# Kernel tuning notes

Hardware: AMD Instinct MI355X
Metric: run time of the kernel (lower is better)

Reference implementation:

```python
import jax, jax.numpy as jnp
import numpy as np
from jax import lax

B, T = 2, 2048
D = 512        # d_model
K = 64         # k_lookback (causal window)


def setup_inputs() -> dict:
    key = jax.random.key(0)
    k1, k2, k3 = jax.random.split(key, 3)
    x = jax.random.normal(k1, (B, 1, T), jnp.float32)
    conv_w = jax.random.normal(k2, (D, 1, 3), jnp.float32) * 0.2
    conv_b = jax.random.normal(k3, (D,), jnp.float32) * 0.05
    gate = jnp.array(0.5, jnp.float32)  # nn.Parameter scalar
    return {"x": x, "conv_w": conv_w, "conv_b": conv_b, "gate": gate}


def reference(x, conv_w, conv_b, gate):
    # feature_proj: Conv1d(1, D, k=3, pad=1) + exact GELU (dropout inactive at eval)
    q = lax.conv_general_dilated(
        x, conv_w, window_strides=(1,), padding=[(1, 1)],
        dimension_numbers=("NCH", "OIH", "NCH"))
    q = jax.nn.gelu(q + conv_b[None, :, None], approximate=False)  # [B, D, T]

    # causal sliding windows: keys_windows[b,c,t,j] = q[b,c, t-(K-1)+j] (0 outside)
    padded = jnp.pad(q, ((0, 0), (0, 0), (K - 1, 0)))
    idx = jnp.arange(T)[:, None] + jnp.arange(K)[None, :]  # [T, K]
    kw = padded[:, :, idx]                                  # [B, D, T, K]

    energy = jnp.einsum("bct,bctk->btk", q, kw)             # [B, T, K]
    attn = jax.nn.softmax(energy / np.float32(np.sqrt(D)), axis=-1)
    context = jnp.einsum("btk,bctk->bct", attn, kw)         # [B, D, T]
    return context * jnp.tanh(gate)
```

## Files before the change

kernel.cpp:

```cpp
#include <hip/hip_runtime.h>
#include <math.h>

#define B 2
#define T 2048
#define D 512
#define KW 64
#define SCALE 0.044194173824159216f

typedef __attribute__((ext_vector_type(8))) short short8;
typedef __attribute__((ext_vector_type(4))) float f32x4;

__device__ __forceinline__ ushort f2bf(float f) {
  union { float f; unsigned u; } v; v.f = f;
  unsigned r = v.u + 0x7fffu + ((v.u >> 16) & 1u);
  return (ushort)(r >> 16);
}

__device__ __forceinline__ float gelu_fast(float v) {
  float v2 = v * v;
  float u  = fmaf(v2 * v, 0.03567740814f, 0.7978845608f * v);
  float e  = __builtin_amdgcn_exp2f(2.885390082f * u);
  float r  = __builtin_amdgcn_rcpf(1.f + e);
  return fmaf(-v, r, v);
}

__device__ __forceinline__ int qt_off(int j, int c) {
  return j * 512 + (c ^ ((j & 7) << 3));
}
__device__ __forceinline__ int qc_off(int c, int j) {
  return (j >> 5) * 16384 + c * 32 + ((j & 31) ^ (((c >> 1) & 3) << 3));
}

__global__ __launch_bounds__(256, 1) void k_fused(
    const float* __restrict__ x, const float* __restrict__ w,
    const float* __restrict__ bias, const float* __restrict__ gate,
    float* __restrict__ out) {
  __shared__ alignas(16) ushort s_q[96 * 512];
  __shared__ alignas(16) f32x4 s_E[4 * 5 * 64];
  __shared__ ushort s_attn[4][16 * 96];

  int blk  = blockIdx.x;
  int b    = blk >> 7;
  int t0   = (blk & 127) << 4;
  int tid  = threadIdx.x;
  int wv   = tid >> 6;
  int lane = tid & 63;
  int n    = lane & 15;
  int quad = lane >> 4;

  int c0 = lane * 8;
  float wf[24], bf[8];
#pragma unroll
  for (int v4 = 0; v4 < 6; ++v4)
    *(float4*)&wf[v4 * 4] = *(const float4*)(w + (size_t)c0 * 3 + v4 * 4);
#pragma unroll
  for (int v4 = 0; v4 < 2; ++v4)
    *(float4*)&bf[v4 * 4] = *(const float4*)(bias + c0 + v4 * 4);
  const float* xb = x + (size_t)b * T;

  for (int it = 0; it < 24; ++it) {
    int j  = wv + it * 4;
    int tp = t0 - 64 + j;
    bool inr = (unsigned)tp < (unsigned)T;
    float xm1 = ((unsigned)(tp - 1) < (unsigned)T) ? xb[tp - 1] : 0.f;
    float x0  = inr                    ? xb[tp]     : 0.f;
    float xp1 = ((unsigned)(tp + 1) < (unsigned)T) ? xb[tp + 1] : 0.f;
    short8 pk;
#pragma unroll
    for (int e = 0; e < 8; ++e) {
      float v = fmaf(xm1, wf[e * 3], fmaf(x0, wf[e * 3 + 1],
                fmaf(xp1, wf[e * 3 + 2], bf[e])));
      pk[e] = inr ? (short)f2bf(gelu_fast(v)) : (short)0;
    }
    *(short8*)&s_q[qt_off(j, c0)] = pk;
  }
  __syncthreads();

  short8 afr[4], bfr[4][5];
#pragma unroll
  for (int i = 0; i < 4; ++i) {
    int cofs = (wv * 4 + i) * 32 + quad * 8;
    afr[i] = *(const short8*)&s_q[qt_off(64 + n, cofs)];
#pragma unroll
    for (int jc = 0; jc < 5; ++jc)
      bfr[i][jc] = *(const short8*)&s_q[qt_off(1 + jc * 16 + n, cofs)];
  }

  f32x4 acc[5];
#pragma unroll
  for (int jc = 0; jc < 5; ++jc) acc[jc] = (f32x4){0.f, 0.f, 0.f, 0.f};
#pragma unroll
  for (int i = 0; i < 4; ++i)
#pragma unroll
    for (int jc = 0; jc < 5; ++jc)
      acc[jc] = __builtin_amdgcn_mfma_f32_16x16x32_bf16(afr[i], bfr[i][jc],
                                                        acc[jc], 0, 0, 0);

#pragma unroll
  for (int jc = 0; jc < 5; ++jc)
    s_E[(wv * 5 + jc) * 64 + lane] = acc[jc];
  __syncthreads();

#pragma unroll
  for (int ww = 0; ww < 4; ++ww) {
    if (ww == wv) continue;
#pragma unroll
    for (int jc = 0; jc < 5; ++jc) {
      f32x4 v = s_E[(ww * 5 + jc) * 64 + lane];
      acc[jc][0] += v[0]; acc[jc][1] += v[1];
      acc[jc][2] += v[2]; acc[jc][3] += v[3];
    }
  }

  ushort* sa = s_attn[wv];
#pragma unroll
  for (int r = 0; r < 4; ++r) {
    int m = quad * 4 + r;
    float e[5];
    float mx = -1e30f;
#pragma unroll
    for (int jc = 0; jc < 5; ++jc) {
      int j = jc * 16 + n;
      bool valid = (j >= m) && (j <= m + (KW - 1));
      e[jc] = valid ? acc[jc][r] * SCALE : -1e30f;
      mx = fmaxf(mx, e[jc]);
    }
#pragma unroll
    for (int off = 1; off <= 8; off <<= 1) mx = fmaxf(mx, __shfl_xor(mx, off, 64));
    float p[5];
    float s = 0.f;
#pragma unroll
    for (int jc = 0; jc < 5; ++jc) {
      p[jc] = (e[jc] > -1e29f) ? __expf(e[jc] - mx) : 0.f;
      s += p[jc];
    }
#pragma unroll
    for (int off = 1; off <= 8; off <<= 1) s += __shfl_xor(s, off, 64);
    float inv = 1.f / s;
#pragma unroll
    for (int jc = 0; jc < 5; ++jc) {
      int j = jc * 16 + n;
      sa[m * 96 + j + 1] = f2bf(p[jc] * inv);
    }
    int jp = (n == 0) ? 0 : (80 + n);
    sa[m * 96 + jp] = 0;
  }
  short8 afr2[3];
#pragma unroll
  for (int ks = 0; ks < 3; ++ks)
    afr2[ks] = *(const short8*)(sa + n * 96 + ks * 32 + quad * 8);

  for (int k = 0; k < 3; ++k) {
    short8 tr[8];
#pragma unroll
    for (int g = 0; g < 8; ++g) {
      int c  = tid + ((g & 1) << 8);
      int j0 = (g >> 1) << 3;
#pragma unroll
      for (int e = 0; e < 8; ++e)
        tr[g][e] = (short)s_q[qt_off(k * 32 + j0 + e, c)];
    }
    __syncthreads();
#pragma unroll
    for (int g = 0; g < 8; ++g) {
      int c  = tid + ((g & 1) << 8);
      int j0 = (g >> 1) << 3;
      *(short8*)&s_q[qc_off(c, k * 32 + j0)] = tr[g];
    }
    __syncthreads();
  }

  const float tg = tanhf(gate[0]);
#pragma unroll
  for (int ncl = 0; ncl < 8; ++ncl) {
    int c = (wv * 8 + ncl) * 16 + n;
    f32x4 co = (f32x4){0.f, 0.f, 0.f, 0.f};
#pragma unroll
    for (int ks = 0; ks < 3; ++ks) {
      short8 bfr2 = *(const short8*)&s_q[qc_off(c, ks * 32 + quad * 8)];
      co = __builtin_amdgcn_mfma_f32_16x16x32_bf16(afr2[ks], bfr2, co, 0, 0, 0);
    }
    f32x4 o;
    o[0] = co[0] * tg; o[1] = co[1] * tg; o[2] = co[2] * tg; o[3] = co[3] * tg;
    *(f32x4*)(out + ((size_t)b * D + c) * T + t0 + quad * 4) = o;
  }
}

extern "C" void kernel_launch(void* const* d_in, const int* in_sizes, int n_in,
                              void* d_out, int out_size, void* d_ws, size_t ws_size,
                              hipStream_t stream) {
  const float* x      = (const float*)d_in[0];
  const float* conv_w = (const float*)d_in[1];
  const float* conv_b = (const float*)d_in[2];
  const float* gate   = (const float*)d_in[3];
  float* out = (float*)d_out;
  (void)d_ws; (void)ws_size;

  k_fused<<<B * T / 16, 256, 0, stream>>>(x, conv_w, conv_b, gate, out);
}
```

Measured before the change: 82.16 us.

## Split conv+GELU into a separate kernel and DMA padded q tiles into LDS

The fused kernel recomputed conv+GELU for 96 rows per 16-row tile, so each q row was computed about six times. The new k_conv kernel computes q once into a zero-padded bf16 workspace. k_attn then loads its window straight into LDS through global_load_lds with the XOR swizzle, and blocks are remapped so neighbouring tiles share an XCD for L2 reuse. The cost is a second launch and a global round trip for q (about 4 MB).

```diff
diff --git a/kernel.cpp b/kernel.cpp
--- a/kernel.cpp
+++ b/kernel.cpp
@@ -6,6 +6,8 @@
 #define D 512
 #define KW 64
 #define SCALE 0.044194173824159216f
+
+#define RQ (64 + T + 16)
 
 typedef __attribute__((ext_vector_type(8))) short short8;
 typedef __attribute__((ext_vector_type(4))) float f32x4;
@@ -24,6 +26,70 @@
   return fmaf(-v, r, v);
 }
 
+__device__ __forceinline__ void gload_lds16(const ushort* gsrc, ushort* lds_dst) {
+  __builtin_amdgcn_global_load_lds(
+      (const __attribute__((address_space(1))) unsigned*)gsrc,
+      (__attribute__((address_space(3))) unsigned*)lds_dst, 16, 0, 0);
+}
+
+__global__ __launch_bounds__(256) void k_conv(
+    const float* __restrict__ x, const float* __restrict__ w,
+    const float* __restrict__ bias, ushort* __restrict__ q) {
+  int blk = blockIdx.x;
+  int tid = threadIdx.x;
+
+  if (blk >= 512) {
+    int ztid = (blk - 512) * 256 + tid;
+    const uint4 z = {0u, 0u, 0u, 0u};
+    for (int task = ztid; task < 10240; task += 2048) {
+      size_t e;
+      if (task < 8192) {
+        int b = task >> 12, i = task & 4095;
+        e = (size_t)b * RQ * D + (size_t)i * 8;
+      } else {
+        int idx = task - 8192;
+        int b = idx >> 10, i = idx & 1023;
+        e = (size_t)b * RQ * D + (size_t)(64 + T) * D + (size_t)i * 8;
+      }
+      *(uint4*)(q + e) = z;
+    }
+    return;
+  }
+
+  int xcd = blk & 7;
+  int i   = blk >> 3;
+  int b   = xcd >> 2;
+  int t0  = (xcd & 3) * 512 + (i >> 3) * 64;
+  int c0  = (i & 7) * 64;
+
+  int lt = tid >> 2;
+  int cb = (tid & 3) << 4;
+  int t = t0 + lt;
+  float xm1 = (t > 0)     ? x[b * T + t - 1] : 0.f;
+  float x0  =               x[b * T + t];
+  float xp1 = (t < T - 1) ? x[b * T + t + 1] : 0.f;
+
+  float wf[48], bf[16];
+#pragma unroll
+  for (int v4 = 0; v4 < 12; ++v4)
+    *(float4*)&wf[v4 * 4] = *(const float4*)(w + (size_t)(c0 + cb) * 3 + v4 * 4);
+#pragma unroll
+  for (int v4 = 0; v4 < 4; ++v4)
+    *(float4*)&bf[v4 * 4] = *(const float4*)(bias + c0 + cb + v4 * 4);
+
+  short8 h0, h1;
+#pragma unroll
+  for (int e = 0; e < 16; ++e) {
+    float v = fmaf(xm1, wf[e * 3], fmaf(x0, wf[e * 3 + 1],
+              fmaf(xp1, wf[e * 3 + 2], bf[e])));
+    float g = gelu_fast(v);
+    if (e < 8) h0[e] = (short)f2bf(g); else h1[e - 8] = (short)f2bf(g);
+  }
+  ushort* qp = q + ((size_t)b * RQ + 64 + t) * D + c0 + cb;
+  *(short8*)qp = h0;
+  *(short8*)(qp + 8) = h1;
+}
+
 __device__ __forceinline__ int qt_off(int j, int c) {
   return j * 512 + (c ^ ((j & 7) << 3));
 }
@@ -31,48 +97,30 @@
   return (j >> 5) * 16384 + c * 32 + ((j & 31) ^ (((c >> 1) & 3) << 3));
 }
 
-__global__ __launch_bounds__(256, 1) void k_fused(
-    const float* __restrict__ x, const float* __restrict__ w,
-    const float* __restrict__ bias, const float* __restrict__ gate,
+__global__ __launch_bounds__(256, 1) void k_attn(
+    const ushort* __restrict__ q, const float* __restrict__ gate,
     float* __restrict__ out) {
   __shared__ alignas(16) ushort s_q[96 * 512];
   __shared__ alignas(16) f32x4 s_E[4 * 5 * 64];
   __shared__ ushort s_attn[4][16 * 96];
 
   int blk  = blockIdx.x;
-  int b    = blk >> 7;
-  int t0   = (blk & 127) << 4;
+  int tile = (blk & 7) * 32 + (blk >> 3);
+  int b    = tile >> 7;
+  int t0   = (tile & 127) << 4;
   int tid  = threadIdx.x;
   int wv   = tid >> 6;
   int lane = tid & 63;
   int n    = lane & 15;
   int quad = lane >> 4;
 
-  int c0 = lane * 8;
-  float wf[24], bf[8];
-#pragma unroll
-  for (int v4 = 0; v4 < 6; ++v4)
-    *(float4*)&wf[v4 * 4] = *(const float4*)(w + (size_t)c0 * 3 + v4 * 4);
-#pragma unroll
-  for (int v4 = 0; v4 < 2; ++v4)
-    *(float4*)&bf[v4 * 4] = *(const float4*)(bias + c0 + v4 * 4);
-  const float* xb = x + (size_t)b * T;
-
+  float g0 = gate[0];
+
+  const ushort* qwin = q + ((size_t)b * RQ + t0) * D;
   for (int it = 0; it < 24; ++it) {
-    int j  = wv + it * 4;
-    int tp = t0 - 64 + j;
-    bool inr = (unsigned)tp < (unsigned)T;
-    float xm1 = ((unsigned)(tp - 1) < (unsigned)T) ? xb[tp - 1] : 0.f;
-    float x0  = inr                    ? xb[tp]     : 0.f;
-    float xp1 = ((unsigned)(tp + 1) < (unsigned)T) ? xb[tp + 1] : 0.f;
-    short8 pk;
-#pragma unroll
-    for (int e = 0; e < 8; ++e) {
-      float v = fmaf(xm1, wf[e * 3], fmaf(x0, wf[e * 3 + 1],
-                fmaf(xp1, wf[e * 3 + 2], bf[e])));
-      pk[e] = inr ? (short)f2bf(gelu_fast(v)) : (short)0;
-    }
-    *(short8*)&s_q[qt_off(j, c0)] = pk;
+    int j = wv + it * 4;
+    gload_lds16(qwin + (size_t)j * D + ((lane ^ (j & 7)) << 3),
+                &s_q[j * 512]);
   }
   __syncthreads();
 
@@ -170,7 +218,7 @@
     __syncthreads();
   }
 
-  const float tg = tanhf(gate[0]);
+  const float tg = tanhf(g0);
 #pragma unroll
   for (int ncl = 0; ncl < 8; ++ncl) {
     int c = (wv * 8 + ncl) * 16 + n;
@@ -194,7 +242,9 @@
   const float* conv_b = (const float*)d_in[2];
   const float* gate   = (const float*)d_in[3];
   float* out = (float*)d_out;
-  (void)d_ws; (void)ws_size;
-
-  k_fused<<<B * T / 16, 256, 0, stream>>>(x, conv_w, conv_b, gate, out);
-}
+
+  ushort* q_ws = (ushort*)d_ws;
+
+  k_conv<<<520, 256, 0, stream>>>(x, conv_w, conv_b, q_ws);
+  k_attn<<<B * T / 16, 256, 0, stream>>>(q_ws, gate, out);
+}
```

After: 73.49 us. 10.6% less time.
